# Kernel optimization log

Hardware: AMD Instinct MI355X
Metric: run time of the kernel (lower is better)

The kernel has to match this reference:

```python
import jax, jax.numpy as jnp
import numpy as np

N, E, D, DH, MH, MO = 100000, 1600000, 128, 512, 512, 128
EPS_BN = 1e-5
EPS_LN = 1e-5


def setup_inputs() -> dict:
    key = jax.random.key(0)
    ks = jax.random.split(key, 16)
    def lin(k, fan_in, shape):
        return jax.random.normal(k, shape, jnp.float32) / np.sqrt(fan_in)
    return {
        'x': jax.random.normal(ks[0], (N, D), jnp.float32),
        'src': jax.random.randint(ks[1], (E,), 0, N, jnp.int32),
        'dst': jax.random.randint(ks[2], (E,), 0, N, jnp.int32),
        'gcn_w': lin(ks[3], D, (D, D)),
        'gcn_b': jnp.zeros((D,), jnp.float32),
        'ff_w1': lin(ks[4], D, (D, DH)),
        'ff_b1': jnp.zeros((DH,), jnp.float32),
        'ln_g': jnp.ones((DH,), jnp.float32),
        'ln_b': jnp.zeros((DH,), jnp.float32),
        'ff_w2': lin(ks[5], DH, (DH, D)),
        'ff_b2': jnp.zeros((D,), jnp.float32),
        'fc1_w': lin(ks[6], D, (D, MH)),
        'fc1_b': jnp.zeros((MH,), jnp.float32),
        'bn1_g': jnp.ones((MH,), jnp.float32),
        'bn1_b': jnp.zeros((MH,), jnp.float32),
        'fc2_w': lin(ks[7], MH, (MH, MH)),
        'fc2_b': jnp.zeros((MH,), jnp.float32),
        'bn2_g': jnp.ones((MH,), jnp.float32),
        'bn2_b': jnp.zeros((MH,), jnp.float32),
        'fc3_w': lin(ks[8], MH, (MH, MO)),
        'fc3_b': jnp.zeros((MO,), jnp.float32),
        'bn3_g': jnp.ones((MO,), jnp.float32),
        'bn3_b': jnp.zeros((MO,), jnp.float32),
        'fc4_w': lin(ks[9], MO, (MO, 1)),
        'fc4_b': jnp.zeros((1,), jnp.float32),
    }


def _gelu(x):
    return jax.nn.gelu(x, approximate=False)  # torch nn.GELU default (erf)


def _batchnorm(x, g, b):
    # BatchNorm1d in training mode: batch statistics, biased variance
    m = jnp.mean(x, axis=0)
    v = jnp.var(x, axis=0)
    return (x - m) * jax.lax.rsqrt(v + EPS_BN) * g + b


def reference(x, src, dst, gcn_w, gcn_b, ff_w1, ff_b1, ln_g, ln_b, ff_w2, ff_b2,
              fc1_w, fc1_b, bn1_g, bn1_b, fc2_w, fc2_b, bn2_g, bn2_b,
              fc3_w, fc3_b, bn3_g, bn3_b, fc4_w, fc4_b):
    n = x.shape[0]
    ones = jnp.ones(src.shape[0], x.dtype)
    out_deg = jnp.clip(jax.ops.segment_sum(ones, src, num_segments=n), 1.0)
    in_deg = jnp.clip(jax.ops.segment_sum(ones, dst, num_segments=n), 1.0)
    # GraphConv, norm='both': left-normalize, aggregate, matmul (in==out), right-normalize, bias
    h = x * (out_deg ** -0.5)[:, None]
    agg = jax.ops.segment_sum(h[src], dst, num_segments=n)  # [N, D]
    h = agg @ gcn_w
    h = h * (in_deg ** -0.5)[:, None] + gcn_b
    # FeedForwardLayer: lin1 -> GELU -> LayerNorm -> lin2
    f = _gelu(h @ ff_w1 + ff_b1)
    mu = jnp.mean(f, axis=-1, keepdims=True)
    var = jnp.var(f, axis=-1, keepdims=True)
    f = (f - mu) * jax.lax.rsqrt(var + EPS_LN) * ln_g + ln_b
    h = f @ ff_w2 + ff_b2  # [N, D]
    # MLP head
    h = _batchnorm(_gelu(h @ fc1_w + fc1_b), bn1_g, bn1_b)
    h = _batchnorm(_gelu(h @ fc2_w + fc2_b), bn2_g, bn2_b)
    h = _batchnorm(_gelu(h @ fc3_w + fc3_b), bn3_g, bn3_b)
    return h @ fc4_w + fc4_b  # [N, 1]
```

## Files before the change

kernel.cpp:

```cpp
#include <hip/hip_runtime.h>
#include <hip/hip_bf16.h>

#define N_NODES 100000
#define NPAD    100096
#define NRB     782
#define E_EDGES 1600000
#define NBLK_SCAN 98

#define HNR  4
#define HP   64
#define HCHK 25000
#define HRSZ 32768

#define AS1 __attribute__((address_space(1)))
#define AS3 __attribute__((address_space(3)))

typedef unsigned int   uint;
typedef unsigned short ushort;
typedef __attribute__((ext_vector_type(8))) short bfx8;
typedef __attribute__((ext_vector_type(4))) float fx4;

__device__ __forceinline__ float bf2f(ushort u) {
    return __uint_as_float(((uint)u) << 16);
}
__device__ __forceinline__ ushort f2bf(float f) {
    uint x = __float_as_uint(f);
    return (ushort)((x + 0x7FFFu + ((x >> 16) & 1u)) >> 16);
}
__device__ __forceinline__ float gelu_fast(float x) {
    float u = 1.5957691f * __builtin_fmaf(0.044715f * x * x, x, x);
    return x / (1.0f + __expf(-u));
}
__device__ __forceinline__ float wave_sum(float v) {
    #pragma unroll
    for (int m = 1; m < 64; m <<= 1) v += __shfl_xor(v, m, 64);
    return v;
}
__device__ __forceinline__ int xcd_swz(int orig, int nwg) {
    int q = nwg >> 3, r = nwg & 7;
    int x = orig & 7, o = orig >> 3;
    return (x < r ? x * (q + 1) : r * (q + 1) + (x - r) * q) + o;
}

__global__ void k_hist(const int* __restrict__ idx, uint* __restrict__ part)
{
    __shared__ uint h[HRSZ / 2];
    int c = blockIdx.x & (HP - 1);
    int r = blockIdx.x / HP;
    int t = threadIdx.x;
    for (int i = t; i < HRSZ / 2; i += 256) h[i] = 0u;
    __syncthreads();
    int base = r << 15;
    int e0 = c * HCHK;
    for (int e = e0 + t; e < e0 + HCHK; e += 256) {
        int v = idx[e] - base;
        if ((uint)v < (uint)HRSZ)
            atomicAdd(&h[v >> 1], 1u << ((v & 1) * 16));
    }
    __syncthreads();
    uint* dst = part + ((size_t)blockIdx.x << 14);
    for (int i = t; i < HRSZ / 2; i += 256) dst[i] = h[i];
}

__global__ void k_degmerge(const uint* __restrict__ partO, const uint* __restrict__ partI,
                           int* __restrict__ inc, float* __restrict__ oscale,
                           float* __restrict__ ininv)
{
    int n = blockIdx.x * 256 + threadIdx.x;
    if (n >= NPAD) return;
    int r = n >> 15, i = (n & 32767) >> 1, hi = (n & 1) * 16;
    const uint* po = partO + ((size_t)(r * HP) << 14) + i;
    const uint* pi = partI + ((size_t)(r * HP) << 14) + i;
    uint so = 0, si = 0;
    for (int c = 0; c < HP; ++c) {
        so += (po[(size_t)c << 14] >> hi) & 0xffffu;
        si += (pi[(size_t)c << 14] >> hi) & 0xffffu;
    }
    inc[n] = (int)si;
    oscale[n] = rsqrtf((float)max((int)so, 1));
    ininv[n] = rsqrtf((float)max((int)si, 1));
}

__global__ void k_scan1(const int* __restrict__ inc, int* __restrict__ coff, int* __restrict__ btot)
{
    __shared__ int a[1024], bsh[1024];
    int t = threadIdx.x;
    int i = blockIdx.x * 1024 + t;
    a[t] = (i < N_NODES) ? inc[i] : 0;
    __syncthreads();
    int* s = a; int* d = bsh;
    for (int dd = 1; dd < 1024; dd <<= 1) {
        int v = s[t] + ((t >= dd) ? s[t - dd] : 0);
        d[t] = v;
        __syncthreads();
        int* tmp = s; s = d; d = tmp;
    }
    if (i < N_NODES) coff[i + 1] = s[t];
    if (t == 1023) btot[blockIdx.x] = s[t];
}

__global__ void k_scan2(int* __restrict__ btot)
{
    __shared__ int a[128], bsh[128];
    int t = threadIdx.x;
    a[t] = (t < NBLK_SCAN) ? btot[t] : 0;
    __syncthreads();
    int* s = a; int* d = bsh;
    for (int dd = 1; dd < 128; dd <<= 1) {
        int v = s[t] + ((t >= dd) ? s[t - dd] : 0);
        d[t] = v;
        __syncthreads();
        int* tmp = s; s = d; d = tmp;
    }
    if (t < NBLK_SCAN) btot[t] = s[t];
}

__global__ void k_scan3(int* __restrict__ coff, const int* __restrict__ btot)
{
    int i = blockIdx.x * 256 + threadIdx.x;
    if (i == 0) coff[0] = 0;
    if (i < N_NODES) {
        int blk = i >> 10;
        if (blk > 0) coff[i + 1] += btot[blk - 1];
    }
}

__global__ void k_fill(const int* __restrict__ src, const int* __restrict__ dst,
                       const int* __restrict__ coff, int* __restrict__ cur, int* __restrict__ eidx)
{
    int e = blockIdx.x * 256 + threadIdx.x;
    if (e < E_EDGES) {
        int d = dst[e];
        int p = coff[d] + atomicAdd(&cur[d], 1);
        eidx[p] = src[e];
    }
}

__global__ void k_xhat(const float* __restrict__ x, const float* __restrict__ oscale,
                       ushort* __restrict__ xh)
{
    size_t i = (size_t)blockIdx.x * 256 + threadIdx.x;
    size_t e0 = i * 4;
    int row = (int)(e0 >> 7);
    uint2 o;
    if (row < N_NODES) {
        float4 v = *(const float4*)(x + e0);
        float s = oscale[row];
        o.x = (uint)f2bf(v.x * s) | ((uint)f2bf(v.y * s) << 16);
        o.y = (uint)f2bf(v.z * s) | ((uint)f2bf(v.w * s) << 16);
    } else {
        o.x = 0u; o.y = 0u;
    }
    *(uint2*)(xh + e0) = o;
}

__global__ void k_agg(const int* __restrict__ off, const int* __restrict__ eidx,
                      const ushort* __restrict__ xh, ushort* __restrict__ agg)
{
    int wid = threadIdx.x >> 6, lane = threadIdx.x & 63;
    int r = blockIdx.x * 4 + wid;
    if (r >= NPAD) return;
    int f = lane & 15;
    int g = lane >> 4;
    float a[8] = {0.f, 0.f, 0.f, 0.f, 0.f, 0.f, 0.f, 0.f};
    if (r < N_NODES) {
        int s = off[r], e = off[r + 1];
        for (int i = s + g; i < e; i += 4) {
            int sv = eidx[i];
            bfx8 v = *(const bfx8*)(xh + (size_t)sv * 128 + f * 8);
            #pragma unroll
            for (int k = 0; k < 8; ++k) a[k] += bf2f((ushort)v[k]);
        }
    }
    #pragma unroll
    for (int k = 0; k < 8; ++k) {
        a[k] += __shfl_xor(a[k], 16, 64);
        a[k] += __shfl_xor(a[k], 32, 64);
    }
    if (g == 0) {
        bfx8 o;
        #pragma unroll
        for (int k = 0; k < 8; ++k) o[k] = (short)f2bf(a[k]);
        *(bfx8*)(agg + (size_t)r * 128 + f * 8) = o;
    }
}

__global__ void k_wT(const float* __restrict__ W, int K, int M, ushort* __restrict__ Wt)
{
    int id = blockIdx.x * 256 + threadIdx.x;
    if (id < K * M) {
        int m = id / K, k = id - m * K;
        Wt[id] = f2bf(W[(size_t)k * M + m]);
    }
}

__global__ void k_wT_ln(const float* __restrict__ W, const float* __restrict__ g,
                        const float* __restrict__ b, const float* __restrict__ b2,
                        ushort* __restrict__ Wt, float* __restrict__ u, float* __restrict__ t)
{
    int wid = threadIdx.x >> 6, lane = threadIdx.x & 63;
    int m = blockIdx.x * 4 + wid;
    if (m >= 128) return;
    float us = 0.f, ts = 0.f;
    for (int k = lane; k < 512; k += 64) {
        float w = W[(size_t)k * 128 + m];
        float gk = g[k], bk = b[k];
        Wt[(size_t)m * 512 + k] = f2bf(gk * w);
        us += gk * w; ts += bk * w;
    }
    us = wave_sum(us); ts = wave_sum(ts);
    if (lane == 0) { u[m] = us; t[m] = ts + b2[m]; }
}

template <int EPI, int STATS>
__global__ __launch_bounds__(256, 4) void k_gemm(
    const ushort* __restrict__ A, const ushort* __restrict__ Bt,
    ushort* __restrict__ C, int K, int M,
    const float* __restrict__ colv0, const float* __restrict__ rowv0,
    const float* __restrict__ rowv1, const float* __restrict__ colv1,
    float* __restrict__ pS, float* __restrict__ pQ, int grb0)
{
    __shared__ __align__(16) char smem[32768 + (STATS == 1 ? 1024 : 0)];
    char* AsB = smem;
    char* BsB = smem + 16384;

    const int nwg = gridDim.x;
    const int wgid = xcd_swz(blockIdx.x, nwg);
    const int nCB = M >> 7;
    const int cb = wgid % nCB;
    const int rb = wgid / nCB;
    const int tid = threadIdx.x;
    const int lane = tid & 63;
    const int wid = tid >> 6;
    const int m0 = (wid >> 1) * 64;
    const int n0 = (wid & 1) * 64;
    const int frl = lane & 15;
    const int kg = lane >> 4;

    float* statsf = (float*)(smem + 32768);
    if (STATS == 1 && tid < 128) { statsf[tid] = 0.f; statsf[128 + tid] = 0.f; }

    fx4 acc[4][4] = {};

    const ushort* Arow0 = A + (size_t)(rb * 128) * K;
    const ushort* Brow0 = Bt + (size_t)(cb * 128) * K;

    for (int kb = 0; kb < K; kb += 64) {
        #pragma unroll
        for (int c = 0; c < 4; ++c) {
            int b = c * 4096 + tid * 16;
            int row = b >> 7;
            int cibs = (b & 127) ^ ((row & 7) << 4);
            const char* ga = (const char*)(Arow0 + (size_t)row * K + kb) + cibs;
            const char* gb = (const char*)(Brow0 + (size_t)row * K + kb) + cibs;
            char* la = AsB + c * 4096 + (wid << 10);
            char* lb = BsB + c * 4096 + (wid << 10);
            __builtin_amdgcn_global_load_lds((const AS1 void*)ga, (AS3 void*)la, 16, 0, 0);
            __builtin_amdgcn_global_load_lds((const AS1 void*)gb, (AS3 void*)lb, 16, 0, 0);
        }
        __syncthreads();
        #pragma unroll
        for (int kk = 0; kk < 2; ++kk) {
            bfx8 av[4], bv[4];
            #pragma unroll
            for (int i = 0; i < 4; ++i) {
                int ar = m0 + i * 16 + frl;
                int ab = (ar * 128 + kk * 64 + kg * 16) ^ ((ar & 7) << 4);
                av[i] = *(const bfx8*)(AsB + ab);
                int br = n0 + i * 16 + frl;
                int bb = (br * 128 + kk * 64 + kg * 16) ^ ((br & 7) << 4);
                bv[i] = *(const bfx8*)(BsB + bb);
            }
            #pragma unroll
            for (int i = 0; i < 4; ++i)
                #pragma unroll
                for (int j = 0; j < 4; ++j)
                    acc[i][j] = __builtin_amdgcn_mfma_f32_16x16x32_bf16(av[i], bv[j], acc[i][j], 0, 0, 0);
        }
        __syncthreads();
    }

    float sL[4] = {0.f, 0.f, 0.f, 0.f}, qL[4] = {0.f, 0.f, 0.f, 0.f};
    #pragma unroll
    for (int j = 0; j < 4; ++j) {
        int colL = n0 + j * 16 + frl;
        float c0 = colv0[cb * 128 + colL];
        float c1 = (EPI == 3) ? colv1[cb * 128 + colL] : 0.f;
        #pragma unroll
        for (int i = 0; i < 4; ++i) {
            int rbaseL = m0 + i * 16 + kg * 4;
            #pragma unroll
            for (int r = 0; r < 4; ++r) {
                float v = acc[i][j][r];
                int rowL = rbaseL + r;
                int grow = (grb0 + rb) * 128 + rowL;
                if (EPI == 0)      v = v * rowv0[grow] + c0;
                else if (EPI == 1) v = gelu_fast(v + c0);
                else if (EPI == 3) v = rowv0[grow] * v + rowv1[grow] * c1 + c0;
                if (STATS == 1) {
                    if (grow < N_NODES) { sL[j] += v; qL[j] += v * v; }
                }
                int boff = rowL * 256 + ((colL * 2) ^ ((rowL & 7) << 4));
                *(ushort*)(smem + boff) = f2bf(v);
            }
        }
    }
    if (STATS == 1) {
        #pragma unroll
        for (int j = 0; j < 4; ++j) {
            float s = sL[j], q = qL[j];
            s += __shfl_xor(s, 16, 64); s += __shfl_xor(s, 32, 64);
            q += __shfl_xor(q, 16, 64); q += __shfl_xor(q, 32, 64);
            if (kg == 0) {
                atomicAdd(&statsf[n0 + j * 16 + frl], s);
                atomicAdd(&statsf[128 + n0 + j * 16 + frl], q);
            }
        }
    }
    __syncthreads();
    {
        int r2 = tid >> 4;
        int s2 = tid & 15;
        #pragma unroll
        for (int pass = 0; pass < 8; ++pass) {
            int rowL = pass * 16 + r2;
            int boff = rowL * 256 + ((s2 * 16) ^ ((rowL & 7) << 4));
            bfx8 v = *(const bfx8*)(smem + boff);
            *(bfx8*)((char*)(C + (size_t)((grb0 + rb) * 128 + rowL - grb0 * 128) * M + cb * 128) + s2 * 16) = v;
        }
    }
    if (STATS == 1 && tid < 128) {
        size_t pidx = ((size_t)(grb0 + rb) * nCB + cb) * 128 + tid;
        pS[pidx] = statsf[tid];
        pQ[pidx] = statsf[128 + tid];
    }
    if (STATS == 2) {
        int rowL = tid >> 1, half = tid & 1;
        float s = 0.f, q = 0.f;
        #pragma unroll
        for (int ss = 0; ss < 8; ++ss) {
            int boff = rowL * 256 + (((half * 64 + ss * 8) * 2) ^ ((rowL & 7) << 4));
            bfx8 v = *(const bfx8*)(smem + boff);
            #pragma unroll
            for (int k2 = 0; k2 < 8; ++k2) {
                float f = bf2f((ushort)v[k2]);
                s += f; q += f * f;
            }
        }
        s += __shfl_xor(s, 1, 64);
        q += __shfl_xor(q, 1, 64);
        if (half == 0) {
            size_t pidx = (size_t)cb * NPAD + (size_t)(grb0 + rb) * 128 + rowL;
            pS[pidx] = s;
            pQ[pidx] = q;
        }
    }
}

__global__ void k_rowmerge(const float* __restrict__ pS, const float* __restrict__ pQ,
                           float* __restrict__ lnS, float* __restrict__ lnC)
{
    int r = blockIdx.x * 256 + threadIdx.x;
    if (r >= NPAD) return;
    float s = 0.f, q = 0.f;
    #pragma unroll
    for (int cb = 0; cb < 4; ++cb) {
        s += pS[(size_t)cb * NPAD + r];
        q += pQ[(size_t)cb * NPAD + r];
    }
    float mean = s * (1.f / 512.f);
    float var = fmaxf(q * (1.f / 512.f) - mean * mean, 0.f);
    float sr = rsqrtf(var + 1e-5f);
    lnS[r] = sr;
    lnC[r] = -mean * sr;
}

__global__ void k_colmerge(const float* __restrict__ pS, const float* __restrict__ pQ,
                           float* __restrict__ oS, float* __restrict__ oQ, int M)
{
    int wid = threadIdx.x >> 6, lane = threadIdx.x & 63;
    int m = blockIdx.x * 4 + wid;
    if (m >= M) return;
    int nCB = M >> 7, cb = m >> 7, colL = m & 127;
    float s = 0.f, q = 0.f;
    for (int rb = lane; rb < NRB; rb += 64) {
        size_t idx = ((size_t)rb * nCB + cb) * 128 + colL;
        s += pS[idx]; q += pQ[idx];
    }
    s = wave_sum(s); q = wave_sum(q);
    if (lane == 0) { oS[m] = s; oQ[m] = q; }
}

__global__ void k_fold(const float* __restrict__ W, const float* __restrict__ bw,
                       const float* __restrict__ g, const float* __restrict__ bb,
                       const float* __restrict__ sum, const float* __restrict__ sqs,
                       int K, int M, ushort* __restrict__ WtO, float* __restrict__ bO)
{
    int wid = threadIdx.x >> 6, lane = threadIdx.x & 63;
    int m = blockIdx.x * 4 + wid;
    if (m >= M) return;
    float acc = 0.f;
    for (int k = lane; k < K; k += 64) {
        float mean = sum[k] * (1.f / (float)N_NODES);
        float var = sqs[k] * (1.f / (float)N_NODES) - mean * mean;
        float s = g[k] * rsqrtf(var + 1e-5f);
        float t = bb[k] - mean * s;
        float w = W[(size_t)k * M + m];
        WtO[(size_t)m * K + k] = f2bf(w * s);
        acc += t * w;
    }
    acc = wave_sum(acc);
    if (lane == 0) bO[m] = bw[m] + acc;
}

__global__ void k_out(const ushort* __restrict__ m3, const ushort* __restrict__ w4,
                      const float* __restrict__ b4, float* __restrict__ out)
{
    int wid = threadIdx.x >> 6, lane = threadIdx.x & 63;
    int r = blockIdx.x * 4 + wid;
    if (r >= N_NODES) return;
    uint u = *(const uint*)(m3 + (size_t)r * 128 + lane * 2);
    uint w = *(const uint*)(w4 + lane * 2);
    float acc = bf2f((ushort)(u & 0xffffu)) * bf2f((ushort)(w & 0xffffu))
              + bf2f((ushort)(u >> 16)) * bf2f((ushort)(w >> 16));
    acc = wave_sum(acc);
    if (lane == 0) out[r] = acc + b4[0];
}

extern "C" void kernel_launch(void* const* d_in, const int* in_sizes, int n_in,
                              void* d_out, int out_size, void* d_ws, size_t ws_size,
                              hipStream_t stream)
{
    const float* x     = (const float*)d_in[0];
    const int*   src   = (const int*)d_in[1];
    const int*   dst   = (const int*)d_in[2];
    const float* gcn_w = (const float*)d_in[3];
    const float* gcn_b = (const float*)d_in[4];
    const float* ff_w1 = (const float*)d_in[5];
    const float* ff_b1 = (const float*)d_in[6];
    const float* ln_g  = (const float*)d_in[7];
    const float* ln_b  = (const float*)d_in[8];
    const float* ff_w2 = (const float*)d_in[9];
    const float* ff_b2 = (const float*)d_in[10];
    const float* fc1_w = (const float*)d_in[11];
    const float* fc1_b = (const float*)d_in[12];
    const float* bn1_g = (const float*)d_in[13];
    const float* bn1_b = (const float*)d_in[14];
    const float* fc2_w = (const float*)d_in[15];
    const float* fc2_b = (const float*)d_in[16];
    const float* bn2_g = (const float*)d_in[17];
    const float* bn2_b = (const float*)d_in[18];
    const float* fc3_w = (const float*)d_in[19];
    const float* fc3_b = (const float*)d_in[20];
    const float* bn3_g = (const float*)d_in[21];
    const float* bn3_b = (const float*)d_in[22];
    const float* fc4_w = (const float*)d_in[23];
    const float* fc4_b = (const float*)d_in[24];
    float* out = (float*)d_out;
    (void)in_sizes; (void)n_in; (void)out_size;

    char* base = (char*)d_ws;
    char* p = base;
    auto alloc = [&](size_t bytes) -> char* {
        char* r = p;
        p += (bytes + 255) & ~(size_t)255;
        return r;
    };
    int*    inc    = (int*)alloc((size_t)NPAD * 4);
    int*    cur    = (int*)alloc((size_t)NPAD * 4);
    int*    coff   = (int*)alloc(((size_t)NPAD + 1) * 4);
    int*    btot   = (int*)alloc(128 * 4);
    int*    eidx   = (int*)alloc((size_t)E_EDGES * 4);
    float*  oscale = (float*)alloc((size_t)NPAD * 4);
    float*  ininv  = (float*)alloc((size_t)NPAD * 4);
    float*  bns    = (float*)alloc(6 * 512 * 4);
    float*  b2p    = (float*)alloc(512 * 4);
    float*  b3p    = (float*)alloc(128 * 4);
    float*  b4p    = (float*)alloc(4);
    float*  lnS    = (float*)alloc((size_t)NPAD * 4);
    float*  lnC    = (float*)alloc((size_t)NPAD * 4);
    float*  lnU    = (float*)alloc(128 * 4);
    float*  lnT    = (float*)alloc(128 * 4);
    float*  pS     = (float*)alloc((size_t)4 * NPAD * 4);
    float*  pQ     = (float*)alloc((size_t)4 * NPAD * 4);
    ushort* gwT    = (ushort*)alloc(128 * 128 * 2);
    ushort* ff1T   = (ushort*)alloc(512 * 128 * 2);
    ushort* ff2T   = (ushort*)alloc(128 * 512 * 2);
    ushort* fc1T   = (ushort*)alloc(512 * 128 * 2);
    ushort* fc2T   = (ushort*)alloc(512 * 512 * 2);
    ushort* fc3T   = (ushort*)alloc(128 * 512 * 2);
    ushort* w4t    = (ushort*)alloc(128 * 2);
    ushort* buf1   = (ushort*)alloc((size_t)NPAD * 128 * 2);
    ushort* bufC   = (ushort*)alloc((size_t)NPAD * 512 * 2);

    size_t used = (size_t)(p - base);
    bool   sep  = (used + (size_t)NPAD * 512 * 2) <= ws_size;
    ushort* m2  = sep ? (ushort*)alloc((size_t)NPAD * 512 * 2) : bufC;

    uint* partO = (uint*)bufC;
    uint* partI = partO + (size_t)HNR * HP * (HRSZ / 2);
    ushort* xh  = bufC;
    ushort* agg = bufC + (size_t)NPAD * 128;

    float* bn1s = bns;
    float* bn1q = bns + 512;
    float* bn2s = bns + 1024;
    float* bn2q = bns + 1536;
    float* bn3s = bns + 2048;
    float* bn3q = bns + 2560;

    hipMemsetAsync(cur, 0, (size_t)NPAD * 4, stream);

    k_hist<<<HNR * HP, 256, 0, stream>>>(src, partO);
    k_hist<<<HNR * HP, 256, 0, stream>>>(dst, partI);
    k_degmerge<<<(NPAD + 255) / 256, 256, 0, stream>>>(partO, partI, inc, oscale, ininv);
    k_scan1<<<NBLK_SCAN, 1024, 0, stream>>>(inc, coff, btot);
    k_scan2<<<1, 128, 0, stream>>>(btot);
    k_scan3<<<(N_NODES + 255) / 256, 256, 0, stream>>>(coff, btot);
    k_fill<<<E_EDGES / 256, 256, 0, stream>>>(src, dst, coff, cur, eidx);
    k_xhat<<<(NPAD / 256) * 32, 256, 0, stream>>>(x, oscale, xh);
    k_agg<<<NPAD / 4, 256, 0, stream>>>(coff, eidx, xh, agg);

    k_wT<<<(128 * 128) / 256, 256, 0, stream>>>(gcn_w, 128, 128, gwT);
    k_wT<<<(128 * 512) / 256, 256, 0, stream>>>(ff_w1, 128, 512, ff1T);
    k_wT<<<(128 * 512) / 256, 256, 0, stream>>>(fc1_w, 128, 512, fc1T);
    k_wT_ln<<<32, 256, 0, stream>>>(ff_w2, ln_g, ln_b, ff_b2, ff2T, lnU, lnT);

    k_gemm<0, 0><<<NRB, 256, 0, stream>>>(agg, gwT, buf1, 128, 128,
                                          gcn_b, ininv, nullptr, nullptr, nullptr, nullptr, 0);
    k_gemm<1, 2><<<4 * NRB, 256, 0, stream>>>(buf1, ff1T, bufC, 128, 512,
                                              ff_b1, nullptr, nullptr, nullptr, pS, pQ, 0);
    k_rowmerge<<<(NPAD + 255) / 256, 256, 0, stream>>>(pS, pQ, lnS, lnC);
    k_gemm<3, 0><<<NRB, 256, 0, stream>>>(bufC, ff2T, buf1, 512, 128,
                                          lnT, lnS, lnC, lnU, nullptr, nullptr, 0);
    k_gemm<1, 1><<<4 * NRB, 256, 0, stream>>>(buf1, fc1T, bufC, 128, 512,
                                              fc1_b, nullptr, nullptr, nullptr, pS, pQ, 0);
    k_colmerge<<<128, 256, 0, stream>>>(pS, pQ, bn1s, bn1q, 512);
    k_fold<<<512 / 4, 256, 0, stream>>>(fc2_w, fc2_b, bn1_g, bn1_b, bn1s, bn1q, 512, 512, fc2T, b2p);
    if (sep) {
        k_gemm<1, 1><<<4 * NRB, 256, 0, stream>>>(bufC, fc2T, m2, 512, 512,
                                                  b2p, nullptr, nullptr, nullptr, pS, pQ, 0);
    } else {
        const int cOff[6] = {0, 195, 390, 585, 780, 782};
        for (int c = 0; c < 5; ++c) {
            int rb0 = cOff[c], nrb = cOff[c + 1] - rb0;
            k_gemm<1, 1><<<nrb * 4, 256, 0, stream>>>(bufC + (size_t)rb0 * 128 * 512, fc2T,
                                                      buf1, 512, 512,
                                                      b2p, nullptr, nullptr, nullptr, pS, pQ, rb0);
            hipMemcpyAsync(bufC + (size_t)rb0 * 128 * 512, buf1,
                           (size_t)nrb * 128 * 512 * 2, hipMemcpyDeviceToDevice, stream);
        }
    }
    k_colmerge<<<128, 256, 0, stream>>>(pS, pQ, bn2s, bn2q, 512);
    k_fold<<<128 / 4, 256, 0, stream>>>(fc3_w, fc3_b, bn2_g, bn2_b, bn2s, bn2q, 512, 128, fc3T, b3p);
    k_gemm<1, 1><<<NRB, 256, 0, stream>>>(m2, fc3T, buf1, 512, 128,
                                          b3p, nullptr, nullptr, nullptr, pS, pQ, 0);
    k_colmerge<<<32, 256, 0, stream>>>(pS, pQ, bn3s, bn3q, 128);
    k_fold<<<1, 256, 0, stream>>>(fc4_w, fc4_b, bn3_g, bn3_b, bn3s, bn3q, 128, 1, w4t, b4p);
    k_out<<<N_NODES / 4, 256, 0, stream>>>(buf1, w4t, b4p, out);
}
```

Measured before the change: 670.7 us.

## Fuse back-to-back 128-wide and 512-wide GEMMs into row-block kernels

Adds a fused kernel that computes a 128-column GEMM per 128-row block, keeps its bf16 result in LDS, and immediately runs the following 512-column GEMM with GELU and statistics. GCN matmul+FF lin1 (with LayerNorm row stats computed in-kernel, removing the rowmerge pass) and FF lin2+fc1 are each merged, so the N×128 intermediates never go to global memory and two launches disappear. In exchange each block uses about 66KB of LDS and fewer blocks run concurrently. The second fused kernel also writes its output into the same buffer it reads from, relying on each block touching only its own rows.

```diff
diff --git a/kernel.cpp b/kernel.cpp
--- a/kernel.cpp
+++ b/kernel.cpp
@@ -212,12 +212,207 @@
     if (lane == 0) { u[m] = us; t[m] = ts + b2[m]; }
 }
 
+template <int K1, int EPI1, int STATS2>
+__global__ __launch_bounds__(256, 2) void k_fused(
+    const ushort* __restrict__ A1, const ushort* __restrict__ B1t,
+    const ushort* __restrict__ B2t, ushort* __restrict__ C,
+    const float* __restrict__ c1v0, const float* __restrict__ r1v0,
+    const float* __restrict__ r1v1, const float* __restrict__ c1v1,
+    const float* __restrict__ bias2,
+    float* __restrict__ lnS, float* __restrict__ lnC,
+    float* __restrict__ pS, float* __restrict__ pQ)
+{
+    __shared__ __align__(16) char smem[32768 + 32768 + 2048];
+    char* A2 = smem;
+    char* S  = smem + 32768;
+    float* st_s = (float*)(smem + 65536);
+    float* st_q = (float*)(smem + 65536 + 1024);
+
+    const int rb = xcd_swz(blockIdx.x, gridDim.x);
+    const int tid = threadIdx.x;
+    const int lane = tid & 63;
+    const int wid = tid >> 6;
+    const int m0 = (wid >> 1) * 64;
+    const int n0 = (wid & 1) * 64;
+    const int frl = lane & 15;
+    const int kg = lane >> 4;
+
+    char* As = S;
+    char* Bs = S + 16384;
+    fx4 acc[4][4] = {};
+    const ushort* Arow0 = A1 + (size_t)(rb * 128) * K1;
+
+    for (int kb = 0; kb < K1; kb += 64) {
+        #pragma unroll
+        for (int c = 0; c < 4; ++c) {
+            int b = c * 4096 + tid * 16;
+            int row = b >> 7;
+            int cibs = (b & 127) ^ ((row & 7) << 4);
+            const char* ga = (const char*)(Arow0 + (size_t)row * K1 + kb) + cibs;
+            const char* gb = (const char*)(B1t + (size_t)row * K1 + kb) + cibs;
+            char* la = As + c * 4096 + (wid << 10);
+            char* lb = Bs + c * 4096 + (wid << 10);
+            __builtin_amdgcn_global_load_lds((const AS1 void*)ga, (AS3 void*)la, 16, 0, 0);
+            __builtin_amdgcn_global_load_lds((const AS1 void*)gb, (AS3 void*)lb, 16, 0, 0);
+        }
+        __syncthreads();
+        #pragma unroll
+        for (int kk = 0; kk < 2; ++kk) {
+            bfx8 av[4], bv[4];
+            #pragma unroll
+            for (int i = 0; i < 4; ++i) {
+                int ar = m0 + i * 16 + frl;
+                int ab = (ar * 128 + kk * 64 + kg * 16) ^ ((ar & 7) << 4);
+                av[i] = *(const bfx8*)(As + ab);
+                int br = n0 + i * 16 + frl;
+                int bb = (br * 128 + kk * 64 + kg * 16) ^ ((br & 7) << 4);
+                bv[i] = *(const bfx8*)(Bs + bb);
+            }
+            #pragma unroll
+            for (int i = 0; i < 4; ++i)
+                #pragma unroll
+                for (int j = 0; j < 4; ++j)
+                    acc[i][j] = __builtin_amdgcn_mfma_f32_16x16x32_bf16(av[i], bv[j], acc[i][j], 0, 0, 0);
+        }
+        __syncthreads();
+    }
+
+    #pragma unroll
+    for (int j = 0; j < 4; ++j) {
+        int colL = n0 + j * 16 + frl;
+        float c0 = c1v0[colL];
+        float c1 = (EPI1 == 3) ? c1v1[colL] : 0.f;
+        #pragma unroll
+        for (int i = 0; i < 4; ++i) {
+            int rbaseL = m0 + i * 16 + kg * 4;
+            #pragma unroll
+            for (int r = 0; r < 4; ++r) {
+                float v = acc[i][j][r];
+                int rowL = rbaseL + r;
+                int grow = rb * 128 + rowL;
+                if (EPI1 == 0) v = v * r1v0[grow] + c0;
+                else           v = r1v0[grow] * v + r1v1[grow] * c1 + c0;
+                *(ushort*)(A2 + rowL * 256 + ((colL * 2) ^ ((rowL & 7) << 4))) = f2bf(v);
+            }
+        }
+    }
+    __syncthreads();
+
+    float rs = 0.f, rq = 0.f;
+    const int rowR = tid >> 1, halfR = tid & 1;
+
+    for (int cb2 = 0; cb2 < 4; ++cb2) {
+        #pragma unroll
+        for (int c = 0; c < 8; ++c) {
+            int b = c * 4096 + tid * 16;
+            int row = b >> 8;
+            int cibs = (b & 255) ^ ((row & 7) << 4);
+            const char* gb = (const char*)(B2t + (size_t)(cb2 * 128 + row) * 128) + cibs;
+            char* lb = S + c * 4096 + (wid << 10);
+            __builtin_amdgcn_global_load_lds((const AS1 void*)gb, (AS3 void*)lb, 16, 0, 0);
+        }
+        __syncthreads();
+
+        fx4 a2[4][4] = {};
+        #pragma unroll
+        for (int kk = 0; kk < 4; ++kk) {
+            bfx8 av[4], bv[4];
+            int c2 = kk * 64 + kg * 16;
+            #pragma unroll
+            for (int i = 0; i < 4; ++i) {
+                int ar = m0 + i * 16 + frl;
+                av[i] = *(const bfx8*)(A2 + ar * 256 + (c2 ^ ((ar & 7) << 4)));
+                int br = n0 + i * 16 + frl;
+                bv[i] = *(const bfx8*)(S + br * 256 + (c2 ^ ((br & 7) << 4)));
+            }
+            #pragma unroll
+            for (int i = 0; i < 4; ++i)
+                #pragma unroll
+                for (int j = 0; j < 4; ++j)
+                    a2[i][j] = __builtin_amdgcn_mfma_f32_16x16x32_bf16(av[i], bv[j], a2[i][j], 0, 0, 0);
+        }
+        __syncthreads();
+
+        float sL[4] = {0.f, 0.f, 0.f, 0.f}, qL[4] = {0.f, 0.f, 0.f, 0.f};
+        #pragma unroll
+        for (int j = 0; j < 4; ++j) {
+            int colL = n0 + j * 16 + frl;
+            float bcol = bias2[cb2 * 128 + colL];
+            #pragma unroll
+            for (int i = 0; i < 4; ++i) {
+                int rbaseL = m0 + i * 16 + kg * 4;
+                #pragma unroll
+                for (int r = 0; r < 4; ++r) {
+                    float v = gelu_fast(a2[i][j][r] + bcol);
+                    int rowL = rbaseL + r;
+                    if (STATS2 == 1) {
+                        if (rb * 128 + rowL < N_NODES) { sL[j] += v; qL[j] += v * v; }
+                    }
+                    *(ushort*)(S + rowL * 256 + ((colL * 2) ^ ((rowL & 7) << 4))) = f2bf(v);
+                }
+            }
+            if (STATS2 == 1) {
+                float s = sL[j], q = qL[j];
+                s += __shfl_xor(s, 16, 64); s += __shfl_xor(s, 32, 64);
+                q += __shfl_xor(q, 16, 64); q += __shfl_xor(q, 32, 64);
+                if (kg == 0) {
+                    st_s[(wid >> 1) * 128 + n0 + j * 16 + frl] = s;
+                    st_q[(wid >> 1) * 128 + n0 + j * 16 + frl] = q;
+                }
+            }
+        }
+        __syncthreads();
+
+        {
+            int r2 = tid >> 4;
+            int s2 = tid & 15;
+            #pragma unroll
+            for (int pass = 0; pass < 8; ++pass) {
+                int rowL = pass * 16 + r2;
+                int boff = rowL * 256 + ((s2 * 16) ^ ((rowL & 7) << 4));
+                bfx8 v = *(const bfx8*)(S + boff);
+                *(bfx8*)((char*)(C + (size_t)(rb * 128 + rowL) * 512 + cb2 * 128) + s2 * 16) = v;
+            }
+        }
+        if (STATS2 == 1 && tid < 128) {
+            size_t pidx = ((size_t)rb * 4 + cb2) * 128 + tid;
+            pS[pidx] = st_s[tid] + st_s[128 + tid];
+            pQ[pidx] = st_q[tid] + st_q[128 + tid];
+        }
+        if (STATS2 == 2) {
+            #pragma unroll
+            for (int ss = 0; ss < 8; ++ss) {
+                int boff = rowR * 256 + (((halfR * 64 + ss * 8) * 2) ^ ((rowR & 7) << 4));
+                bfx8 v = *(const bfx8*)(S + boff);
+                #pragma unroll
+                for (int k2 = 0; k2 < 8; ++k2) {
+                    float f = bf2f((ushort)v[k2]);
+                    rs += f; rq += f * f;
+                }
+            }
+        }
+        __syncthreads();
+    }
+
+    if (STATS2 == 2) {
+        rs += __shfl_xor(rs, 1, 64);
+        rq += __shfl_xor(rq, 1, 64);
+        if (halfR == 0) {
+            float mean = rs * (1.f / 512.f);
+            float var = fmaxf(rq * (1.f / 512.f) - mean * mean, 0.f);
+            float sr = rsqrtf(var + 1e-5f);
+            int grow = rb * 128 + rowR;
+            lnS[grow] = sr;
+            lnC[grow] = -mean * sr;
+        }
+    }
+}
+
 template <int EPI, int STATS>
 __global__ __launch_bounds__(256, 4) void k_gemm(
     const ushort* __restrict__ A, const ushort* __restrict__ Bt,
     ushort* __restrict__ C, int K, int M,
     const float* __restrict__ colv0, const float* __restrict__ rowv0,
-    const float* __restrict__ rowv1, const float* __restrict__ colv1,
     float* __restrict__ pS, float* __restrict__ pQ, int grb0)
 {
     __shared__ __align__(16) char smem[32768 + (STATS == 1 ? 1024 : 0)];
@@ -285,7 +480,6 @@
     for (int j = 0; j < 4; ++j) {
         int colL = n0 + j * 16 + frl;
         float c0 = colv0[cb * 128 + colL];
-        float c1 = (EPI == 3) ? colv1[cb * 128 + colL] : 0.f;
         #pragma unroll
         for (int i = 0; i < 4; ++i) {
             int rbaseL = m0 + i * 16 + kg * 4;
@@ -294,9 +488,8 @@
                 float v = acc[i][j][r];
                 int rowL = rbaseL + r;
                 int grow = (grb0 + rb) * 128 + rowL;
-                if (EPI == 0)      v = v * rowv0[grow] + c0;
-                else if (EPI == 1) v = gelu_fast(v + c0);
-                else if (EPI == 3) v = rowv0[grow] * v + rowv1[grow] * c1 + c0;
+                if (EPI == 0) v = v * rowv0[grow] + c0;
+                else          v = gelu_fast(v + c0);
                 if (STATS == 1) {
                     if (grow < N_NODES) { sL[j] += v; qL[j] += v * v; }
                 }
@@ -326,7 +519,7 @@
             int rowL = pass * 16 + r2;
             int boff = rowL * 256 + ((s2 * 16) ^ ((rowL & 7) << 4));
             bfx8 v = *(const bfx8*)(smem + boff);
-            *(bfx8*)((char*)(C + (size_t)((grb0 + rb) * 128 + rowL - grb0 * 128) * M + cb * 128) + s2 * 16) = v;
+            *(bfx8*)((char*)(C + (size_t)(rb * 128 + rowL) * M + cb * 128) + s2 * 16) = v;
         }
     }
     if (STATS == 1 && tid < 128) {
@@ -334,45 +527,6 @@
         pS[pidx] = statsf[tid];
         pQ[pidx] = statsf[128 + tid];
     }
-    if (STATS == 2) {
-        int rowL = tid >> 1, half = tid & 1;
-        float s = 0.f, q = 0.f;
-        #pragma unroll
-        for (int ss = 0; ss < 8; ++ss) {
-            int boff = rowL * 256 + (((half * 64 + ss * 8) * 2) ^ ((rowL & 7) << 4));
-            bfx8 v = *(const bfx8*)(smem + boff);
-            #pragma unroll
-            for (int k2 = 0; k2 < 8; ++k2) {
-                float f = bf2f((ushort)v[k2]);
-                s += f; q += f * f;
-            }
-        }
-        s += __shfl_xor(s, 1, 64);
-        q += __shfl_xor(q, 1, 64);
-        if (half == 0) {
-            size_t pidx = (size_t)cb * NPAD + (size_t)(grb0 + rb) * 128 + rowL;
-            pS[pidx] = s;
-            pQ[pidx] = q;
-        }
-    }
-}
-
-__global__ void k_rowmerge(const float* __restrict__ pS, const float* __restrict__ pQ,
-                           float* __restrict__ lnS, float* __restrict__ lnC)
-{
-    int r = blockIdx.x * 256 + threadIdx.x;
-    if (r >= NPAD) return;
-    float s = 0.f, q = 0.f;
-    #pragma unroll
-    for (int cb = 0; cb < 4; ++cb) {
-        s += pS[(size_t)cb * NPAD + r];
-        q += pQ[(size_t)cb * NPAD + r];
-    }
-    float mean = s * (1.f / 512.f);
-    float var = fmaxf(q * (1.f / 512.f) - mean * mean, 0.f);
-    float sr = rsqrtf(var + 1e-5f);
-    lnS[r] = sr;
-    lnC[r] = -mean * sr;
 }
 
 __global__ void k_colmerge(const float* __restrict__ pS, const float* __restrict__ pQ,
@@ -500,7 +654,7 @@
     uint* partO = (uint*)bufC;
     uint* partI = partO + (size_t)HNR * HP * (HRSZ / 2);
     ushort* xh  = bufC;
-    ushort* agg = bufC + (size_t)NPAD * 128;
+    ushort* agg = buf1;
 
     float* bn1s = bns;
     float* bn1q = bns + 512;
@@ -526,27 +680,24 @@
     k_wT<<<(128 * 512) / 256, 256, 0, stream>>>(fc1_w, 128, 512, fc1T);
     k_wT_ln<<<32, 256, 0, stream>>>(ff_w2, ln_g, ln_b, ff_b2, ff2T, lnU, lnT);
 
-    k_gemm<0, 0><<<NRB, 256, 0, stream>>>(agg, gwT, buf1, 128, 128,
-                                          gcn_b, ininv, nullptr, nullptr, nullptr, nullptr, 0);
-    k_gemm<1, 2><<<4 * NRB, 256, 0, stream>>>(buf1, ff1T, bufC, 128, 512,
-                                              ff_b1, nullptr, nullptr, nullptr, pS, pQ, 0);
-    k_rowmerge<<<(NPAD + 255) / 256, 256, 0, stream>>>(pS, pQ, lnS, lnC);
-    k_gemm<3, 0><<<NRB, 256, 0, stream>>>(bufC, ff2T, buf1, 512, 128,
-                                          lnT, lnS, lnC, lnU, nullptr, nullptr, 0);
-    k_gemm<1, 1><<<4 * NRB, 256, 0, stream>>>(buf1, fc1T, bufC, 128, 512,
-                                              fc1_b, nullptr, nullptr, nullptr, pS, pQ, 0);
+    k_fused<128, 0, 2><<<NRB, 256, 0, stream>>>(agg, gwT, ff1T, bufC,
+                                                gcn_b, ininv, nullptr, nullptr, ff_b1,
+                                                lnS, lnC, nullptr, nullptr);
+    k_fused<512, 3, 1><<<NRB, 256, 0, stream>>>(bufC, ff2T, fc1T, bufC,
+                                                lnT, lnS, lnC, lnU, fc1_b,
+                                                nullptr, nullptr, pS, pQ);
     k_colmerge<<<128, 256, 0, stream>>>(pS, pQ, bn1s, bn1q, 512);
     k_fold<<<512 / 4, 256, 0, stream>>>(fc2_w, fc2_b, bn1_g, bn1_b, bn1s, bn1q, 512, 512, fc2T, b2p);
     if (sep) {
         k_gemm<1, 1><<<4 * NRB, 256, 0, stream>>>(bufC, fc2T, m2, 512, 512,
-                                                  b2p, nullptr, nullptr, nullptr, pS, pQ, 0);
+                                                  b2p, nullptr, pS, pQ, 0);
     } else {
         const int cOff[6] = {0, 195, 390, 585, 780, 782};
         for (int c = 0; c < 5; ++c) {
             int rb0 = cOff[c], nrb = cOff[c + 1] - rb0;
             k_gemm<1, 1><<<nrb * 4, 256, 0, stream>>>(bufC + (size_t)rb0 * 128 * 512, fc2T,
                                                       buf1, 512, 512,
-                                                      b2p, nullptr, nullptr, nullptr, pS, pQ, rb0);
+                                                      b2p, nullptr, pS, pQ, rb0);
             hipMemcpyAsync(bufC + (size_t)rb0 * 128 * 512, buf1,
                            (size_t)nrb * 128 * 512 * 2, hipMemcpyDeviceToDevice, stream);
         }
@@ -554,7 +705,7 @@
     k_colmerge<<<128, 256, 0, stream>>>(pS, pQ, bn2s, bn2q, 512);
     k_fold<<<128 / 4, 256, 0, stream>>>(fc3_w, fc3_b, bn2_g, bn2_b, bn2s, bn2q, 512, 128, fc3T, b3p);
     k_gemm<1, 1><<<NRB, 256, 0, stream>>>(m2, fc3T, buf1, 512, 128,
-                                          b3p, nullptr, nullptr, nullptr, pS, pQ, 0);
+                                          b3p, nullptr, pS, pQ, 0);
     k_colmerge<<<32, 256, 0, stream>>>(pS, pQ, bn3s, bn3q, 128);
     k_fold<<<1, 256, 0, stream>>>(fc4_w, fc4_b, bn3_g, bn3_b, bn3s, bn3q, 128, 1, w4t, b4p);
     k_out<<<N_NODES / 4, 256, 0, stream>>>(buf1, w4t, b4p, out);
```

Measured after the change: 679.1 us. No clear change (+1.3%).
